# Optimization experiments

Measured on AMD Instinct MI355X. Metric: run time of the kernel, lower is better.

Reference implementation:

```python
import jax, jax.numpy as jnp
import numpy as np

B, IN, T, E, S, K, W, HD = 4096, 512, 10, 16, 2, 4, 1024, 64


def setup_inputs() -> dict:
    key = jax.random.key(0)
    ks = jax.random.split(key, 12)
    he = lambda k, shp, fan: jax.random.normal(k, shp, jnp.float32) * (2.0 / fan) ** 0.5
    x = jax.random.normal(ks[0], (B, IN + T), jnp.float32)
    return {
        'x': x,
        'gk': he(ks[1], (T, E), T),
        'rk0': he(ks[2], (E, IN, W), IN),
        'rb0': jax.random.normal(ks[3], (E, W), jnp.float32) * 0.01,
        'rk1': he(ks[4], (E, W, W), W),
        'rb1': jax.random.normal(ks[5], (E, W), jnp.float32) * 0.01,
        'sk0': he(ks[6], (S, IN, W), IN),
        'sb0': jax.random.normal(ks[7], (S, W), jnp.float32) * 0.01,
        'sk1': he(ks[8], (S, W, W), W),
        'sb1': jax.random.normal(ks[9], (S, W), jnp.float32) * 0.01,
        'hk': he(ks[10], (T, W, HD), W),
        'hb': jax.random.normal(ks[11], (T, HD), jnp.float32) * 0.01,
    }


def reference(x, gk, rk0, rb0, rk1, rb1, sk0, sb0, sk1, sb1, hk, hb):
    task_idx = x[:, -T:]            # (B, T) task one-hot / features
    feat = x[:, :-T]                # (B, IN)

    # --- top-k routing on task features ---
    gating_logits = task_idx @ gk                       # (B, E)
    topk_idx = jnp.argsort(-gating_logits, axis=-1)[:, :K]  # (B, K)
    topk_logits = jnp.take_along_axis(gating_logits, topk_idx, axis=-1)
    topk_weights = jax.nn.softmax(topk_logits, axis=-1)     # (B, K)

    # --- routed experts: run every expert chain densely, gather at the end ---
    # h: (B, E, d); each expert's independent MLP chain over the same input.
    h = jnp.broadcast_to(feat[:, None, :], (B, E, IN))
    h = jax.nn.relu(jnp.einsum('bei,eij->bej', h, rk0) + rb0[None])  # (B, E, W)
    h = jax.nn.relu(jnp.einsum('bei,eij->bej', h, rk1) + rb1[None])  # (B, E, W)
    h_sel = jnp.take_along_axis(h, topk_idx[:, :, None], axis=1)     # (B, K, W)
    routed = jnp.einsum('bkw,bk->bw', h_sel, topk_weights)           # (B, W)

    # --- shared experts: all run, mean-combined ---
    hs = jnp.broadcast_to(feat[:, None, :], (B, S, IN))
    hs = jax.nn.relu(jnp.einsum('bsi,sij->bsj', hs, sk0) + sb0[None])
    hs = jax.nn.relu(jnp.einsum('bsi,sij->bsj', hs, sk1) + sb1[None])
    shared = hs.mean(axis=1)                                         # (B, W)

    features_out = jnp.tanh(routed + shared)                         # (B, W)

    # --- per-task heads, select by task id ---
    heads_out = jnp.einsum('bw,twd->btd', features_out, hk) + hb[None]  # (B, T, HD)
    task_indices = task_idx.argmax(axis=-1)                             # (B,)
    out = jnp.take_along_axis(heads_out, task_indices[:, None, None], axis=1)[:, 0]
    return out
```

## Files before the change

### kernel.cpp

```cpp
#include <hip/hip_runtime.h>

typedef unsigned short u16;
typedef __attribute__((ext_vector_type(8))) short bf16x8;
typedef __attribute__((ext_vector_type(4))) float f32x4;

constexpr int B_ = 4096, IN_ = 512, T_ = 10, E_ = 16, S_ = 2, K_ = 4, W_ = 1024, HD_ = 64;
constexpr int XROW = IN_ + T_;
constexpr int NPAIR = B_ * (K_ + S_);
constexpr int MTU = 208;
constexpr int GEMM_GRID = MTU * 8;
constexpr int GB_ = 16;


#define GLL16(g, l) __builtin_amdgcn_global_load_lds( \
    (const __attribute__((address_space(1))) void*)(g), \
    (__attribute__((address_space(3))) void*)(l), 16, 0, 0)

__device__ __forceinline__ u16 f2bf(float x) {
    unsigned u = __float_as_uint(x);
    return (u16)((u + 0x7fffu + ((u >> 16) & 1u)) >> 16);
}
__device__ __forceinline__ float bf2f(u16 b) { return __uint_as_float(((unsigned)b) << 16); }

__global__ __launch_bounds__(256) void featconv(const float* __restrict__ x, u16* __restrict__ featb) {
    int i = blockIdx.x * 256 + threadIdx.x;
    int b = i >> 8;
    int c2 = (i & 255) * 2;
    float2 v = *(const float2*)(x + (size_t)b * XROW + c2);
    ushort2 o;
    o.x = f2bf(v.x);
    o.y = f2bf(v.y);
    *(ushort2*)(featb + (size_t)b * IN_ + c2) = o;
}

__global__ __launch_bounds__(256) void gate_kernel(const float* __restrict__ x, const float* __restrict__ gk,
                                                   int* __restrict__ top4p, float* __restrict__ w6,
                                                   int* __restrict__ task_id, int* __restrict__ blockcounts) {
    __shared__ float sgk[T_ * E_];
    __shared__ int hist[E_];
    int blk = blockIdx.x, tid = threadIdx.x;
    int b = blk * 256 + tid;
    if (tid < T_ * E_) sgk[tid] = gk[tid];
    if (tid < E_) hist[tid] = 0;
    __syncthreads();
    float tv[T_];
#pragma unroll
    for (int i = 0; i < T_; ++i) tv[i] = x[(size_t)b * XROW + IN_ + i];
    float lg[E_];
#pragma unroll
    for (int e = 0; e < E_; ++e) {
        float s = 0.f;
#pragma unroll
        for (int i = 0; i < T_; ++i) s += tv[i] * sgk[i * E_ + e];
        lg[e] = s;
    }
    int idx[K_]; float val[K_];
#pragma unroll
    for (int k = 0; k < K_; ++k) {
        int bi = 0; float bv = -1e30f;
#pragma unroll
        for (int e = 0; e < E_; ++e)
            if (lg[e] > bv) { bv = lg[e]; bi = e; }
        idx[k] = bi; val[k] = bv; lg[bi] = -1e30f;
    }
    float m = val[0];
    float ex[K_]; float s = 0.f;
#pragma unroll
    for (int k = 0; k < K_; ++k) { ex[k] = expf(val[k] - m); s += ex[k]; }
    float inv = 1.f / s;
#pragma unroll
    for (int k = 0; k < K_; ++k) {
        int lp = atomicAdd(&hist[idx[k]], 1);
        top4p[b * K_ + k] = idx[k] | (lp << 8);
        w6[b * 6 + k] = ex[k] * inv;
    }
    w6[b * 6 + 4] = 0.5f;
    w6[b * 6 + 5] = 0.5f;
    int ti = 0; float tb = tv[0];
#pragma unroll
    for (int i = 1; i < T_; ++i)
        if (tv[i] > tb) { tb = tv[i]; ti = i; }
    task_id[b] = ti;
    __syncthreads();
    if (tid < E_) blockcounts[blk * E_ + tid] = hist[tid];
}

__global__ void build_tables(const int* __restrict__ blockcounts, int* __restrict__ meta,
                             int* __restrict__ blockbase) {
    if (threadIdx.x != 0) return;
    int counts[E_];
    for (int e = 0; e < E_; ++e) {
        int s = 0;
        for (int blk = 0; blk < GB_; ++blk) s += blockcounts[blk * E_ + e];
        counts[e] = s;
        meta[e] = s;
    }
    int a = 0;
    for (int e = 0; e < E_; ++e) { meta[16 + e] = a; a += counts[e]; }
    for (int e = 0; e < E_; ++e) {
        int run = meta[16 + e];
        for (int blk = 0; blk < GB_; ++blk) { blockbase[blk * E_ + e] = run; run += blockcounts[blk * E_ + e]; }
    }
    int t = 0;
    for (int g = 0; g < 18; ++g) { meta[48 + g] = t; int c = (g < 16) ? counts[g] : B_; t += (c + 127) >> 7; }
    meta[66] = t;
}

__global__ __launch_bounds__(256) void scatter_kernel(const int* __restrict__ top4p,
                                                      const int* __restrict__ blockbase,
                                                      int* __restrict__ pair_sample, int* __restrict__ pair_dst) {
    int blk = blockIdx.x, tid = threadIdx.x;
    int b = blk * 256 + tid;
#pragma unroll
    for (int k = 0; k < K_; ++k) {
        int v = top4p[b * K_ + k];
        int e = v & 0xFF, lp = v >> 8;
        int p = blockbase[blk * E_ + e] + lp;
        pair_sample[p] = b;
        pair_dst[p] = b * 6 + k;
    }
    pair_sample[B_ * K_ + b] = b;       pair_dst[B_ * K_ + b] = b * 6 + 4;
    pair_sample[B_ * K_ + B_ + b] = b;  pair_dst[B_ * K_ + B_ + b] = b * 6 + 5;
}

__global__ __launch_bounds__(256) void convbf16(const float* __restrict__ in, u16* __restrict__ out) {
    int i = blockIdx.x * 256 + threadIdx.x;
    float4 v = ((const float4*)in)[i];
    ushort4 o;
    o.x = f2bf(v.x); o.y = f2bf(v.y); o.z = f2bf(v.z); o.w = f2bf(v.w);
    ((ushort4*)out)[i] = o;
}

__global__ __launch_bounds__(256) void transconv2(const float* __restrict__ srcA, const float* __restrict__ srcB,
                                                  int splitZ, u16* __restrict__ out, int K, int N) {
    __shared__ float tile[32][33];
    int z = blockIdx.z;
    const float* src = (z < splitZ) ? (srcA + (size_t)z * K * N) : (srcB + (size_t)(z - splitZ) * K * N);
    int k0 = blockIdx.y * 32, n0 = blockIdx.x * 32;
    int tid = threadIdx.x;
    int r = tid >> 3, c4 = (tid & 7) * 4;
    float4 v = *(const float4*)(src + (size_t)(k0 + r) * N + n0 + c4);
    tile[r][c4 + 0] = v.x; tile[r][c4 + 1] = v.y; tile[r][c4 + 2] = v.z; tile[r][c4 + 3] = v.w;
    __syncthreads();
    ushort4 ov;
    ov.x = f2bf(tile[c4 + 0][r]);
    ov.y = f2bf(tile[c4 + 1][r]);
    ov.z = f2bf(tile[c4 + 2][r]);
    ov.w = f2bf(tile[c4 + 3][r]);
    *(ushort4*)(out + (size_t)z * N * K + (size_t)(n0 + r) * K + k0 + c4) = ov;
}

template <int K, int LAYER>
__global__ __launch_bounds__(256, 2) void gemm3(const u16* __restrict__ Asrc, const u16* __restrict__ wT,
                                                const float* __restrict__ rbias, const float* __restrict__ sbias,
                                                const int* __restrict__ pair_sample, const int* __restrict__ pair_dst,
                                                const int* __restrict__ meta, u16* __restrict__ outp) {
    __shared__ char lds[65536];
    int p = blockIdx.x;
    int lid = (p & 7) * (GEMM_GRID >> 3) + (p >> 3);
    int mtu = lid >> 3, nt = lid & 7;
    const int* tpre = meta + 48;
    if (mtu >= tpre[18]) return;
    int e = 0;
    while (mtu >= tpre[e + 1]) ++e;
    int mt = mtu - tpre[e];
    int off, cnt;
    if (e < E_) { off = meta[16 + e]; cnt = meta[e]; }
    else        { off = B_ * K_ + (e - E_) * B_; cnt = B_; }

    const int tid = threadIdx.x;
    const int srow = tid >> 3, sc = tid & 7;
    const u16* wTe = wT + (size_t)e * W_ * K;
    const u16* ab[4];
    const u16* bb[4];
#pragma unroll
    for (int r = 0; r < 4; ++r) {
        int row = r * 32 + srow;
        int swz = (sc ^ (row & 7)) * 8;
        int gm = mt * 128 + row;
        if (gm >= cnt) gm = cnt - 1;
        int arow = (LAYER == 1) ? pair_sample[off + gm] : (off + gm);
        ab[r] = Asrc + (size_t)arow * K + swz;
        bb[r] = wTe + (size_t)(nt * 128 + row) * K + swz;
    }

    auto STAGE = [&](int kt, int buf) {
        char* base = lds + buf * 32768;
#pragma unroll
        for (int r = 0; r < 4; ++r) GLL16(ab[r] + kt * 64, base + r * 4096 + tid * 16);
#pragma unroll
        for (int r = 0; r < 4; ++r) GLL16(bb[r] + kt * 64, base + 16384 + r * 4096 + tid * 16);
    };

    f32x4 acc[4][4];
#pragma unroll
    for (int i = 0; i < 4; ++i)
#pragma unroll
        for (int j = 0; j < 4; ++j) acc[i][j] = (f32x4){0.f, 0.f, 0.f, 0.f};

    const int lane = tid & 63, wid = tid >> 6;
    const int wr = wid >> 1, wc = wid & 1;
    const int fr = lane & 15;
    const int fkb = (lane >> 4) * 16;

    constexpr int NKT = K / 64;
    STAGE(0, 0);
    for (int kt = 0; kt < NKT; ++kt) {
        int cur = kt & 1;
        if (kt + 1 < NKT) {
            STAGE(kt + 1, cur ^ 1);
            asm volatile("s_waitcnt vmcnt(8)" ::: "memory");
        } else {
            asm volatile("s_waitcnt vmcnt(0)" ::: "memory");
        }
        __builtin_amdgcn_s_barrier();
        asm volatile("" ::: "memory");
        char* A = lds + cur * 32768;
        char* Bv = A + 16384;
#pragma unroll
        for (int kk = 0; kk < 2; ++kk) {
            bf16x8 af[4], bf[4];
#pragma unroll
            for (int i = 0; i < 4; ++i) {
                int arow = wr * 64 + i * 16 + fr;
                af[i] = *(const bf16x8*)(A + arow * 128 + ((kk * 64 + fkb) ^ ((arow & 7) << 4)));
                int brow = wc * 64 + i * 16 + fr;
                bf[i] = *(const bf16x8*)(Bv + brow * 128 + ((kk * 64 + fkb) ^ ((brow & 7) << 4)));
            }
            __builtin_amdgcn_s_setprio(1);
#pragma unroll
            for (int i = 0; i < 4; ++i)
#pragma unroll
                for (int j = 0; j < 4; ++j)
                    acc[i][j] = __builtin_amdgcn_mfma_f32_16x16x32_bf16(af[i], bf[j], acc[i][j], 0, 0, 0);
            __builtin_amdgcn_s_setprio(0);
        }
        asm volatile("" ::: "memory");
        __builtin_amdgcn_s_barrier();
    }

    const float* bias = (e < E_) ? (rbias + (size_t)e * W_) : (sbias + (size_t)(e - E_) * W_);
    const int colbase = nt * 128 + wc * 64;
#pragma unroll
    for (int i = 0; i < 4; ++i) {
#pragma unroll
        for (int reg = 0; reg < 4; ++reg) {
            int rowt = wr * 64 + i * 16 + (lane >> 4) * 4 + reg;
            int m = mt * 128 + rowt;
            if (m < cnt) {
                int outrow = (LAYER == 1) ? (off + m) : pair_dst[off + m];
#pragma unroll
                for (int j = 0; j < 4; ++j) {
                    int col = colbase + j * 16 + fr;
                    float v = acc[i][j][reg] + bias[col];
                    outp[(size_t)outrow * W_ + col] = f2bf(fmaxf(v, 0.f));
                }
            }
        }
    }
}

__global__ __launch_bounds__(256) void combine_head(const u16* __restrict__ h2, const float* __restrict__ w6,
                                                    const int* __restrict__ task_id, const u16* __restrict__ hkb,
                                                    const float* __restrict__ hb, float* __restrict__ out) {
    __shared__ float f[W_];
    __shared__ float partials[256];
    int b = blockIdx.x, tid = threadIdx.x;
    float wsl[6];
#pragma unroll
    for (int s = 0; s < 6; ++s) wsl[s] = w6[b * 6 + s];
    int t = task_id[b];
    float sum[4] = {0.f, 0.f, 0.f, 0.f};
#pragma unroll
    for (int s = 0; s < 6; ++s) {
        ushort4 v = *(const ushort4*)(h2 + (size_t)(b * 6 + s) * W_ + tid * 4);
        sum[0] += wsl[s] * bf2f(v.x);
        sum[1] += wsl[s] * bf2f(v.y);
        sum[2] += wsl[s] * bf2f(v.z);
        sum[3] += wsl[s] * bf2f(v.w);
    }
#pragma unroll
    for (int i = 0; i < 4; ++i) f[tid * 4 + i] = tanhf(sum[i]);
    __syncthreads();
    int d = tid & 63, g = tid >> 6;
    const u16* hp = hkb + (size_t)t * W_ * HD_ + d;
    float acc = 0.f;
#pragma unroll 8
    for (int w = g; w < W_; w += 4) acc += f[w] * bf2f(hp[(size_t)w * HD_]);
    partials[tid] = acc;
    __syncthreads();
    if (tid < 64)
        out[(size_t)b * HD_ + tid] =
            partials[tid] + partials[tid + 64] + partials[tid + 128] + partials[tid + 192] + hb[t * HD_ + tid];
}

extern "C" void kernel_launch(void* const* d_in, const int* in_sizes, int n_in,
                              void* d_out, int out_size, void* d_ws, size_t ws_size,
                              hipStream_t stream) {
    const float* x   = (const float*)d_in[0];
    const float* gk  = (const float*)d_in[1];
    const float* rk0 = (const float*)d_in[2];
    const float* rb0 = (const float*)d_in[3];
    const float* rk1 = (const float*)d_in[4];
    const float* rb1 = (const float*)d_in[5];
    const float* sk0 = (const float*)d_in[6];
    const float* sb0 = (const float*)d_in[7];
    const float* sk1 = (const float*)d_in[8];
    const float* sb1 = (const float*)d_in[9];
    const float* hk  = (const float*)d_in[10];
    const float* hb  = (const float*)d_in[11];
    float* out = (float*)d_out;
    (void)in_sizes; (void)n_in; (void)out_size; (void)ws_size;

    char* ws = (char*)d_ws;
    size_t o = 0;
    auto alloc = [&](size_t bytes) { char* p = ws + o; o += (bytes + 255) & ~(size_t)255; return p; };
    int* meta        = (int*)alloc(512);
    int* blockcounts = (int*)alloc((size_t)GB_ * E_ * 4);
    int* blockbase   = (int*)alloc((size_t)GB_ * E_ * 4);
    int* top4p       = (int*)alloc((size_t)B_ * K_ * 4);
    float* w6        = (float*)alloc((size_t)B_ * 6 * 4);
    int* task_id     = (int*)alloc((size_t)B_ * 4);
    int* pair_sample = (int*)alloc((size_t)NPAIR * 4);
    int* pair_dst    = (int*)alloc((size_t)NPAIR * 4);
    u16* featb       = (u16*)alloc((size_t)B_ * IN_ * 2);
    u16* w0T         = (u16*)alloc((size_t)(E_ + S_) * W_ * IN_ * 2);
    u16* w1T         = (u16*)alloc((size_t)(E_ + S_) * W_ * W_ * 2);
    u16* hkb         = (u16*)alloc((size_t)T_ * W_ * HD_ * 2);
    u16* h1          = (u16*)alloc((size_t)NPAIR * W_ * 2);
    u16* h2          = (u16*)alloc((size_t)NPAIR * W_ * 2);

    featconv<<<B_, 256, 0, stream>>>(x, featb);
    gate_kernel<<<GB_, 256, 0, stream>>>(x, gk, top4p, w6, task_id, blockcounts);
    build_tables<<<1, 64, 0, stream>>>(blockcounts, meta, blockbase);
    scatter_kernel<<<GB_, 256, 0, stream>>>(top4p, blockbase, pair_sample, pair_dst);
    transconv2<<<dim3(W_ / 32, IN_ / 32, E_ + S_), 256, 0, stream>>>(rk0, sk0, E_, w0T, IN_, W_);
    transconv2<<<dim3(W_ / 32, W_ / 32, E_ + S_), 256, 0, stream>>>(rk1, sk1, E_, w1T, W_, W_);
    convbf16<<<(T_ * W_ * HD_) / 1024, 256, 0, stream>>>(hk, hkb);
    gemm3<IN_, 1><<<GEMM_GRID, 256, 0, stream>>>(featb, w0T, rb0, sb0, pair_sample, pair_dst, meta, h1);
    gemm3<W_, 2><<<GEMM_GRID, 256, 0, stream>>>(h1, w1T, rb1, sb1, pair_sample, pair_dst, meta, h2);
    combine_head<<<B_, 256, 0, stream>>>(h2, w6, task_id, hkb, hb, out);
}
```

Before: 219.0 us.

## Group head samples by task, stage GEMM epilogue through LDS, rebalance XCD mapping

```diff
diff --git a/kernel.cpp b/kernel.cpp
--- a/kernel.cpp
+++ b/kernel.cpp
@@ -10,6 +10,7 @@
 constexpr int MTU = 208;
 constexpr int GEMM_GRID = MTU * 8;
 constexpr int GB_ = 16;
+constexpr int CB_GRID = 1034;
 
 
 #define GLL16(g, l) __builtin_amdgcn_global_load_lds( \
@@ -35,13 +36,16 @@
 
 __global__ __launch_bounds__(256) void gate_kernel(const float* __restrict__ x, const float* __restrict__ gk,
                                                    int* __restrict__ top4p, float* __restrict__ w6,
-                                                   int* __restrict__ task_id, int* __restrict__ blockcounts) {
+                                                   int* __restrict__ task_id, int* __restrict__ tpp,
+                                                   int* __restrict__ bct_e, int* __restrict__ bct_t) {
     __shared__ float sgk[T_ * E_];
     __shared__ int hist[E_];
+    __shared__ int thist[T_];
     int blk = blockIdx.x, tid = threadIdx.x;
     int b = blk * 256 + tid;
     if (tid < T_ * E_) sgk[tid] = gk[tid];
     if (tid < E_) hist[tid] = 0;
+    if (tid < T_) thist[tid] = 0;
     __syncthreads();
     float tv[T_];
 #pragma unroll
@@ -81,17 +85,20 @@
     for (int i = 1; i < T_; ++i)
         if (tv[i] > tb) { tb = tv[i]; ti = i; }
     task_id[b] = ti;
-    __syncthreads();
-    if (tid < E_) blockcounts[blk * E_ + tid] = hist[tid];
-}
-
-__global__ void build_tables(const int* __restrict__ blockcounts, int* __restrict__ meta,
-                             int* __restrict__ blockbase) {
+    tpp[b] = atomicAdd(&thist[ti], 1);
+    __syncthreads();
+    if (tid < E_) bct_e[blk * E_ + tid] = hist[tid];
+    if (tid < T_) bct_t[blk * T_ + tid] = thist[tid];
+}
+
+__global__ void build_tables(const int* __restrict__ bct_e, const int* __restrict__ bct_t,
+                             int* __restrict__ meta, int* __restrict__ blockbase,
+                             int* __restrict__ tblockbase) {
     if (threadIdx.x != 0) return;
     int counts[E_];
     for (int e = 0; e < E_; ++e) {
         int s = 0;
-        for (int blk = 0; blk < GB_; ++blk) s += blockcounts[blk * E_ + e];
+        for (int blk = 0; blk < GB_; ++blk) s += bct_e[blk * E_ + e];
         counts[e] = s;
         meta[e] = s;
     }
@@ -99,16 +106,38 @@
     for (int e = 0; e < E_; ++e) { meta[16 + e] = a; a += counts[e]; }
     for (int e = 0; e < E_; ++e) {
         int run = meta[16 + e];
-        for (int blk = 0; blk < GB_; ++blk) { blockbase[blk * E_ + e] = run; run += blockcounts[blk * E_ + e]; }
+        for (int blk = 0; blk < GB_; ++blk) { blockbase[blk * E_ + e] = run; run += bct_e[blk * E_ + e]; }
     }
     int t = 0;
     for (int g = 0; g < 18; ++g) { meta[48 + g] = t; int c = (g < 16) ? counts[g] : B_; t += (c + 127) >> 7; }
     meta[66] = t;
+    int tcnt[T_];
+    for (int i = 0; i < T_; ++i) {
+        int s = 0;
+        for (int blk = 0; blk < GB_; ++blk) s += bct_t[blk * T_ + i];
+        tcnt[i] = s;
+        meta[91 + i] = s;
+    }
+    int pr = 0, br = 0;
+    for (int i = 0; i < T_; ++i) {
+        meta[70 + i] = pr;
+        meta[80 + i] = br;
+        pr += ((tcnt[i] + 3) >> 2) << 2;
+        br += (tcnt[i] + 3) >> 2;
+    }
+    meta[90] = br;
+    for (int i = 0; i < T_; ++i) {
+        int run = meta[70 + i];
+        for (int blk = 0; blk < GB_; ++blk) { tblockbase[blk * T_ + i] = run; run += bct_t[blk * T_ + i]; }
+    }
 }
 
 __global__ __launch_bounds__(256) void scatter_kernel(const int* __restrict__ top4p,
                                                       const int* __restrict__ blockbase,
-                                                      int* __restrict__ pair_sample, int* __restrict__ pair_dst) {
+                                                      const int* __restrict__ task_id, const int* __restrict__ tpp,
+                                                      const int* __restrict__ tblockbase,
+                                                      int* __restrict__ pair_sample, int* __restrict__ pair_dst,
+                                                      int* __restrict__ torder) {
     int blk = blockIdx.x, tid = threadIdx.x;
     int b = blk * 256 + tid;
 #pragma unroll
@@ -121,6 +150,7 @@
     }
     pair_sample[B_ * K_ + b] = b;       pair_dst[B_ * K_ + b] = b * 6 + 4;
     pair_sample[B_ * K_ + B_ + b] = b;  pair_dst[B_ * K_ + B_ + b] = b * 6 + 5;
+    torder[tblockbase[blk * T_ + task_id[b]] + tpp[b]] = b;
 }
 
 __global__ __launch_bounds__(256) void convbf16(const float* __restrict__ in, u16* __restrict__ out) {
@@ -156,11 +186,14 @@
                                                 const int* __restrict__ pair_sample, const int* __restrict__ pair_dst,
                                                 const int* __restrict__ meta, u16* __restrict__ outp) {
     __shared__ char lds[65536];
+    const int* tpre = meta + 48;
+    const int nwg = tpre[18] * 8;
     int p = blockIdx.x;
-    int lid = (p & 7) * (GEMM_GRID >> 3) + (p >> 3);
+    if (p >= nwg) return;
+    int q = nwg >> 3, r8 = nwg & 7;
+    int xcd = p & 7, iofs = p >> 3;
+    int lid = (xcd < r8 ? xcd * (q + 1) : r8 * (q + 1) + (xcd - r8) * q) + iofs;
     int mtu = lid >> 3, nt = lid & 7;
-    const int* tpre = meta + 48;
-    if (mtu >= tpre[18]) return;
     int e = 0;
     while (mtu >= tpre[e + 1]) ++e;
     int mt = mtu - tpre[e];
@@ -239,59 +272,92 @@
         __builtin_amdgcn_s_barrier();
     }
 
+    __syncthreads();
     const float* bias = (e < E_) ? (rbias + (size_t)e * W_) : (sbias + (size_t)(e - E_) * W_);
-    const int colbase = nt * 128 + wc * 64;
 #pragma unroll
     for (int i = 0; i < 4; ++i) {
 #pragma unroll
         for (int reg = 0; reg < 4; ++reg) {
-            int rowt = wr * 64 + i * 16 + (lane >> 4) * 4 + reg;
-            int m = mt * 128 + rowt;
-            if (m < cnt) {
-                int outrow = (LAYER == 1) ? (off + m) : pair_dst[off + m];
-#pragma unroll
-                for (int j = 0; j < 4; ++j) {
-                    int col = colbase + j * 16 + fr;
-                    float v = acc[i][j][reg] + bias[col];
-                    outp[(size_t)outrow * W_ + col] = f2bf(fmaxf(v, 0.f));
-                }
+            int r = wr * 64 + i * 16 + (lane >> 4) * 4 + reg;
+#pragma unroll
+            for (int j = 0; j < 4; ++j) {
+                int c = wc * 64 + j * 16 + fr;
+                float v = acc[i][j][reg] + bias[nt * 128 + c];
+                *(u16*)(lds + r * 272 + c * 2) = f2bf(fmaxf(v, 0.f));
             }
         }
     }
-}
-
-__global__ __launch_bounds__(256) void combine_head(const u16* __restrict__ h2, const float* __restrict__ w6,
-                                                    const int* __restrict__ task_id, const u16* __restrict__ hkb,
-                                                    const float* __restrict__ hb, float* __restrict__ out) {
-    __shared__ float f[W_];
-    __shared__ float partials[256];
-    int b = blockIdx.x, tid = threadIdx.x;
-    float wsl[6];
-#pragma unroll
-    for (int s = 0; s < 6; ++s) wsl[s] = w6[b * 6 + s];
-    int t = task_id[b];
-    float sum[4] = {0.f, 0.f, 0.f, 0.f};
-#pragma unroll
-    for (int s = 0; s < 6; ++s) {
-        ushort4 v = *(const ushort4*)(h2 + (size_t)(b * 6 + s) * W_ + tid * 4);
-        sum[0] += wsl[s] * bf2f(v.x);
-        sum[1] += wsl[s] * bf2f(v.y);
-        sum[2] += wsl[s] * bf2f(v.z);
-        sum[3] += wsl[s] * bf2f(v.w);
-    }
-#pragma unroll
-    for (int i = 0; i < 4; ++i) f[tid * 4 + i] = tanhf(sum[i]);
+    __syncthreads();
+#pragma unroll
+    for (int rr = 0; rr < 8; ++rr) {
+        int flat = rr * 4096 + tid * 16;
+        int r = flat >> 8;
+        int co = flat & 255;
+        int m = mt * 128 + r;
+        if (m < cnt) {
+            int outrow = (LAYER == 1) ? (off + m) : pair_dst[off + m];
+            bf16x8 v = *(const bf16x8*)(lds + r * 272 + co);
+            *(bf16x8*)(outp + (size_t)outrow * W_ + nt * 128 + (co >> 1)) = v;
+        }
+    }
+}
+
+__global__ __launch_bounds__(256) void combine4(const u16* __restrict__ h2, const float* __restrict__ w6,
+                                                const int* __restrict__ torder, const int* __restrict__ meta,
+                                                const u16* __restrict__ hkb, const float* __restrict__ hb,
+                                                float* __restrict__ out) {
+    __shared__ float f[4][W_];
+    __shared__ float partials[4][4][64];
+    const int* bp = meta + 80;
+    int blk = blockIdx.x;
+    if (blk >= bp[T_]) return;
+    int t = 0;
+    while (blk >= bp[t + 1]) ++t;
+    int slot0 = meta[70 + t] + (blk - bp[t]) * 4;
+    int vend  = meta[70 + t] + meta[91 + t];
+    int tid = threadIdx.x;
+    int s0 = torder[slot0];
+    int smp[4];
+#pragma unroll
+    for (int i = 0; i < 4; ++i) {
+        int v = torder[slot0 + i];
+        smp[i] = (slot0 + i < vend) ? v : s0;
+    }
+#pragma unroll
+    for (int s = 0; s < 4; ++s) {
+        int b = smp[s];
+        float wsl[6];
+#pragma unroll
+        for (int q = 0; q < 6; ++q) wsl[q] = w6[b * 6 + q];
+        float sum[4] = {0.f, 0.f, 0.f, 0.f};
+#pragma unroll
+        for (int q = 0; q < 6; ++q) {
+            ushort4 v = *(const ushort4*)(h2 + (size_t)(b * 6 + q) * W_ + tid * 4);
+            sum[0] += wsl[q] * bf2f(v.x);
+            sum[1] += wsl[q] * bf2f(v.y);
+            sum[2] += wsl[q] * bf2f(v.z);
+            sum[3] += wsl[q] * bf2f(v.w);
+        }
+#pragma unroll
+        for (int i = 0; i < 4; ++i) f[s][tid * 4 + i] = tanhf(sum[i]);
+    }
     __syncthreads();
     int d = tid & 63, g = tid >> 6;
     const u16* hp = hkb + (size_t)t * W_ * HD_ + d;
-    float acc = 0.f;
-#pragma unroll 8
-    for (int w = g; w < W_; w += 4) acc += f[w] * bf2f(hp[(size_t)w * HD_]);
-    partials[tid] = acc;
-    __syncthreads();
-    if (tid < 64)
-        out[(size_t)b * HD_ + tid] =
-            partials[tid] + partials[tid + 64] + partials[tid + 128] + partials[tid + 192] + hb[t * HD_ + tid];
+    float acc[4] = {0.f, 0.f, 0.f, 0.f};
+#pragma unroll 4
+    for (int w = g; w < W_; w += 4) {
+        float hv = bf2f(hp[(size_t)w * HD_]);
+#pragma unroll
+        for (int s = 0; s < 4; ++s) acc[s] += f[s][w] * hv;
+    }
+#pragma unroll
+    for (int s = 0; s < 4; ++s) partials[g][s][d] = acc[s];
+    __syncthreads();
+    int ss = tid >> 6, dd = tid & 63;
+    float r = partials[0][ss][dd] + partials[1][ss][dd] + partials[2][ss][dd] + partials[3][ss][dd]
+            + hb[t * HD_ + dd];
+    out[(size_t)smp[ss] * HD_ + dd] = r;
 }
 
 extern "C" void kernel_launch(void* const* d_in, const int* in_sizes, int n_in,
@@ -316,13 +382,17 @@
     size_t o = 0;
     auto alloc = [&](size_t bytes) { char* p = ws + o; o += (bytes + 255) & ~(size_t)255; return p; };
     int* meta        = (int*)alloc(512);
-    int* blockcounts = (int*)alloc((size_t)GB_ * E_ * 4);
+    int* bct_e       = (int*)alloc((size_t)GB_ * E_ * 4);
+    int* bct_t       = (int*)alloc((size_t)GB_ * T_ * 4);
     int* blockbase   = (int*)alloc((size_t)GB_ * E_ * 4);
+    int* tblockbase  = (int*)alloc((size_t)GB_ * T_ * 4);
     int* top4p       = (int*)alloc((size_t)B_ * K_ * 4);
     float* w6        = (float*)alloc((size_t)B_ * 6 * 4);
     int* task_id     = (int*)alloc((size_t)B_ * 4);
+    int* tpp         = (int*)alloc((size_t)B_ * 4);
     int* pair_sample = (int*)alloc((size_t)NPAIR * 4);
     int* pair_dst    = (int*)alloc((size_t)NPAIR * 4);
+    int* torder      = (int*)alloc((size_t)(B_ + 64) * 4);
     u16* featb       = (u16*)alloc((size_t)B_ * IN_ * 2);
     u16* w0T         = (u16*)alloc((size_t)(E_ + S_) * W_ * IN_ * 2);
     u16* w1T         = (u16*)alloc((size_t)(E_ + S_) * W_ * W_ * 2);
@@ -331,13 +401,14 @@
     u16* h2          = (u16*)alloc((size_t)NPAIR * W_ * 2);
 
     featconv<<<B_, 256, 0, stream>>>(x, featb);
-    gate_kernel<<<GB_, 256, 0, stream>>>(x, gk, top4p, w6, task_id, blockcounts);
-    build_tables<<<1, 64, 0, stream>>>(blockcounts, meta, blockbase);
-    scatter_kernel<<<GB_, 256, 0, stream>>>(top4p, blockbase, pair_sample, pair_dst);
+    gate_kernel<<<GB_, 256, 0, stream>>>(x, gk, top4p, w6, task_id, tpp, bct_e, bct_t);
+    build_tables<<<1, 64, 0, stream>>>(bct_e, bct_t, meta, blockbase, tblockbase);
+    scatter_kernel<<<GB_, 256, 0, stream>>>(top4p, blockbase, task_id, tpp, tblockbase,
+                                            pair_sample, pair_dst, torder);
     transconv2<<<dim3(W_ / 32, IN_ / 32, E_ + S_), 256, 0, stream>>>(rk0, sk0, E_, w0T, IN_, W_);
     transconv2<<<dim3(W_ / 32, W_ / 32, E_ + S_), 256, 0, stream>>>(rk1, sk1, E_, w1T, W_, W_);
     convbf16<<<(T_ * W_ * HD_) / 1024, 256, 0, stream>>>(hk, hkb);
     gemm3<IN_, 1><<<GEMM_GRID, 256, 0, stream>>>(featb, w0T, rb0, sb0, pair_sample, pair_dst, meta, h1);
     gemm3<W_, 2><<<GEMM_GRID, 256, 0, stream>>>(h1, w1T, rb1, sb1, pair_sample, pair_dst, meta, h2);
-    combine_head<<<B_, 256, 0, stream>>>(h2, w6, task_id, hkb, hb, out);
-}
+    combine4<<<CB_GRID, 256, 0, stream>>>(h2, w6, torder, meta, hkb, hb, out);
+}
```

Result: faster. 204.5 us (-6.6%).
